# Optimization experiments

Hardware: AMD Instinct MI355X
Metric: run time of the kernel (lower is better)

## Reference

```python
import jax, jax.numpy as jnp
import numpy as np

WIN = 7


def rel_index(win: int) -> jnp.ndarray:
    ys, xs = jnp.meshgrid(jnp.arange(win), jnp.arange(win), indexing='ij')
    coords = jnp.stack([ys.reshape(-1), xs.reshape(-1)], axis=-1)  # (S, 2)
    diff = coords[None, :, :] - coords[:, None, :] + (win - 1)     # (S, S, 2)
    return diff[..., 0] * (2 * win - 1) + diff[..., 1]             # (S, S)


def setup_inputs() -> dict:
    key = jax.random.key(0)
    ks = jax.random.split(key, 5)
    B, WN, S, C, H = 64, 64, WIN * WIN, 192, 6
    X = jax.random.normal(ks[0], (B, WN, S, C), dtype=jnp.float32)
    # torch nn.Linear(emb_dim, 3*emb_dim) -> store as (in, out) for x @ W
    Wqkv = jax.random.normal(ks[1], (C, 3 * C), dtype=jnp.float32) * 0.02
    bqkv = jnp.zeros((3 * C,), dtype=jnp.float32)
    Wo = jax.random.normal(ks[2], (C, C), dtype=jnp.float32) * 0.02
    bo = jnp.zeros((C,), dtype=jnp.float32)
    bias_table = jax.random.normal(ks[3], ((2 * WIN - 1) ** 2, H), dtype=jnp.float32) * 0.02
    return {"X": X, "Wqkv": Wqkv, "bqkv": bqkv, "Wo": Wo, "bo": bo, "bias_table": bias_table}


def reference(X, Wqkv, bqkv, Wo, bo, bias_table):
    B, WN, S, C = X.shape
    H = bias_table.shape[1]
    D = C // H
    scale = D ** -0.5
    # qkv projection: (B, WN, S, 3C) -> (3, B, WN, H, S, D)
    qkv = (X @ Wqkv + bqkv).reshape(B, WN, S, 3, H, D).transpose(3, 0, 1, 4, 2, 5)
    q, k, v = qkv[0], qkv[1], qkv[2]
    attn = jnp.einsum('bwhqd,bwhkd->bwhqk', q, k) * scale  # (B, WN, H, S, S)
    # gathered relative position bias: (S, S, H) -> (H, S, S)
    idx = rel_index(WIN)
    bias = bias_table[idx].transpose(2, 0, 1)
    attn = attn + bias[None, None]
    proba = jax.nn.softmax(attn, axis=-1)  # dropout omitted (eval mode)
    out = jnp.einsum('bwhqk,bwhkd->bwhqd', proba, v)  # (B, WN, H, S, D)
    out = out.transpose(0, 1, 3, 2, 4).reshape(B, WN, S, C)
    return out @ Wo + bo
```

## Files before the change

### kernel.cpp

```cpp
#include <hip/hip_runtime.h>
#include <hip/hip_bf16.h>


typedef __attribute__((ext_vector_type(4))) float f32x4;
typedef __attribute__((ext_vector_type(8))) short bf16x8;
typedef __attribute__((ext_vector_type(4))) unsigned short u16x4;

#define SCALE 0.17677669529663689f
#define MFMA(a, b, acc) __builtin_amdgcn_mfma_f32_16x16x32_bf16(a, b, acc, 0, 0, 0)

__device__ __forceinline__ unsigned short f2bf(float f) {
  union { float f; unsigned int u; } v; v.f = f;
  return (unsigned short)((v.u + 0x7FFFu + ((v.u >> 16) & 1u)) >> 16);
}

__global__ void wprep(const float* __restrict__ Wqkv, const float* __restrict__ Wo,
                      unsigned short* __restrict__ WqkvT, unsigned short* __restrict__ WoT) {
  int i = blockIdx.x * 256 + threadIdx.x;
  if (i < 576 * 192) { int n = i / 192, k = i % 192; WqkvT[i] = f2bf(Wqkv[k * 576 + n]); }
  if (i < 192 * 192) { int n = i / 192, k = i % 192; WoT[i]   = f2bf(Wo[k * 192 + n]); }
}

__global__ __launch_bounds__(512, 4)
void qkv_gemm(const float* __restrict__ X, const unsigned short* __restrict__ WqkvT,
              const float* __restrict__ bqkv, unsigned short* __restrict__ qkv) {
  __shared__ __align__(16) unsigned short Bs[2][64 * 200];
  __shared__ __align__(16) unsigned short scr[8][16 * 72];

  const int tid = threadIdx.x, w8 = tid >> 6, lane = tid & 63;
  const int g = lane >> 4, c = lane & 15;
  const size_t bm = (size_t)blockIdx.x * 128;
  const f32x4 z = {0.f, 0.f, 0.f, 0.f};

  bf16x8 af[6];
  {
    const float* xr = X + (bm + w8 * 16 + c) * 192;
    #pragma unroll
    for (int ks = 0; ks < 6; ++ks) {
      f32x4 lo = *(const f32x4*)(xr + ks * 32 + g * 8);
      f32x4 hi = *(const f32x4*)(xr + ks * 32 + g * 8 + 4);
      bf16x8 a;
      a[0] = (short)f2bf(lo[0]); a[1] = (short)f2bf(lo[1]);
      a[2] = (short)f2bf(lo[2]); a[3] = (short)f2bf(lo[3]);
      a[4] = (short)f2bf(hi[0]); a[5] = (short)f2bf(hi[1]);
      a[6] = (short)f2bf(hi[2]); a[7] = (short)f2bf(hi[3]);
      af[ks] = a;
    }
  }

  uint4 st[3];
  #pragma unroll
  for (int jj = 0; jj < 3; ++jj) {
    int j = tid + jj * 512;
    st[jj] = *(const uint4*)(WqkvT + (j / 24) * 192 + (j % 24) * 8);
  }
  #pragma unroll
  for (int jj = 0; jj < 3; ++jj) {
    int j = tid + jj * 512;
    *(uint4*)(&Bs[0][(j / 24) * 200 + (j % 24) * 8]) = st[jj];
  }
  __syncthreads();

  unsigned short* sw = scr[w8];
  for (int nc = 0; nc < 9; ++nc) {
    const int cur = nc & 1;
    if (nc < 8) {
      #pragma unroll
      for (int jj = 0; jj < 3; ++jj) {
        int j = tid + jj * 512;
        st[jj] = *(const uint4*)(WqkvT + (nc + 1) * 12288 + (j / 24) * 192 + (j % 24) * 8);
      }
    }
    f32x4 acc[4] = {z, z, z, z};
    #pragma unroll
    for (int ks = 0; ks < 6; ++ks) {
      const unsigned short* bp = &Bs[cur][c * 200 + ks * 32 + g * 8];
      #pragma unroll
      for (int nf = 0; nf < 4; ++nf)
        acc[nf] = MFMA(af[ks], *(const bf16x8*)(bp + nf * 16 * 200), acc[nf]);
    }
    #pragma unroll
    for (int nf = 0; nf < 4; ++nf) {
      const float bb = bqkv[nc * 64 + nf * 16 + c];
      #pragma unroll
      for (int r = 0; r < 4; ++r)
        sw[(4 * g + r) * 72 + nf * 16 + c] = f2bf(acc[nf][r] + bb);
    }
    uint4 o0 = *(const uint4*)(sw + c * 72 + g * 8);
    uint4 o1 = *(const uint4*)(sw + c * 72 + 32 + g * 8);
    unsigned short* qp = qkv + (bm + w8 * 16 + c) * 576 + nc * 64;
    *(uint4*)(qp + g * 8)      = o0;
    *(uint4*)(qp + 32 + g * 8) = o1;

    if (nc < 8) {
      #pragma unroll
      for (int jj = 0; jj < 3; ++jj) {
        int j = tid + jj * 512;
        *(uint4*)(&Bs[cur ^ 1][(j / 24) * 200 + (j % 24) * 8]) = st[jj];
      }
    }
    __syncthreads();
  }
}

__global__ __launch_bounds__(512, 4)
void attn_win(unsigned short* __restrict__ qkv, const float* __restrict__ btab) {
  __shared__ __align__(16) unsigned short Ks[64 * 200];
  __shared__ __align__(16) unsigned short Vt[192 * 72];
  __shared__ __align__(16) unsigned short scr[8][1152];
  __shared__ float biasF[1014];

  const int tid = threadIdx.x, w8 = tid >> 6, lane = tid & 63;
  const int g = lane >> 4, c = lane & 15;
  const int mt = w8 & 3, hw = w8 >> 2;
  const size_t tokbase = (size_t)blockIdx.x * 49;
  const f32x4 z = {0.f, 0.f, 0.f, 0.f};

  for (int j = tid; j < 1014; j += 512) biasF[j] = btab[j];
  for (int j = tid; j < 360; j += 512) {
    uint4 zz = {0, 0, 0, 0};
    *(uint4*)(&Ks[(49 + j / 24) * 200 + (j % 24) * 8]) = zz;
  }
  for (int j = tid; j < 2880; j += 512) Vt[(j / 15) * 72 + 49 + j % 15] = 0;
  for (int j = tid; j < 1176; j += 512) {
    int row = j / 24, ch = j % 24;
    *(uint4*)(&Ks[row * 200 + ch * 8]) =
        *(const uint4*)(qkv + (tokbase + row) * 576 + 192 + ch * 8);
  }
  for (int j = tid; j < 1176; j += 512) {
    int row = j / 24, ch = j % 24;
    uint4 v = *(const uint4*)(qkv + (tokbase + row) * 576 + 384 + ch * 8);
    const unsigned short* e = (const unsigned short*)&v;
    #pragma unroll
    for (int k = 0; k < 8; ++k) Vt[(ch * 8 + k) * 72 + row] = e[k];
  }
  __syncthreads();

  const int qbase = mt * 16;
  const int q = qbase + c;
  const bool qvalid = q < 49;
  const int qc = qvalid ? q : 48;
  const int qoff6 = ((6 - qc / 7) * 13 + (6 - qc % 7)) * 6;
  int kb6[16];
  #pragma unroll
  for (int i = 0; i < 16; ++i) {
    int k = (i >> 2) * 16 + g * 4 + (i & 3);
    int kk = k < 49 ? k : 48;
    kb6[i] = ((kk / 7) * 13 + (kk % 7)) * 6;
  }
  unsigned short* Pw = scr[w8];

  for (int hi = 0; hi < 3; ++hi) {
    const int h = hw * 3 + hi;
    const bf16x8 bq = *(const bf16x8*)(qkv + (tokbase + qc) * 576 + h * 32 + g * 8);
    const int cofs = h * 32 + g * 8;
    f32x4 s0 = MFMA(*(const bf16x8*)(Ks + (c) * 200 + cofs), bq, z);
    f32x4 s1 = MFMA(*(const bf16x8*)(Ks + (16 + c) * 200 + cofs), bq, z);
    f32x4 s2 = MFMA(*(const bf16x8*)(Ks + (32 + c) * 200 + cofs), bq, z);
    f32x4 s3 = MFMA(*(const bf16x8*)(Ks + (48 + c) * 200 + cofs), bq, z);

    float p[16];
    float mx = -3e38f;
    #pragma unroll
    for (int i = 0; i < 16; ++i) {
      const int t = i >> 2, r = i & 3;
      const int k = t * 16 + g * 4 + r;
      const float sv = (t == 0) ? s0[r] : (t == 1) ? s1[r] : (t == 2) ? s2[r] : s3[r];
      const float b = biasF[kb6[i] + qoff6 + h];
      const float lg = (qvalid && (k < 49)) ? fmaf(sv, SCALE, b) : -1e30f;
      p[i] = lg;
      mx = fmaxf(mx, lg);
    }
    mx = fmaxf(mx, __shfl_xor(mx, 16));
    mx = fmaxf(mx, __shfl_xor(mx, 32));
    float sum = 0.f;
    #pragma unroll
    for (int i = 0; i < 16; ++i) { p[i] = __expf(p[i] - mx); sum += p[i]; }
    sum += __shfl_xor(sum, 16);
    sum += __shfl_xor(sum, 32);
    const float inv = 1.0f / sum;
    #pragma unroll
    for (int t = 0; t < 4; ++t) {
      u16x4 pk;
      #pragma unroll
      for (int r = 0; r < 4; ++r) pk[r] = f2bf(p[t * 4 + r] * inv);
      *(u16x4*)(Pw + c * 72 + t * 16 + g * 4) = pk;
    }

    f32x4 o0 = z, o1 = z;
    #pragma unroll
    for (int ks = 0; ks < 2; ++ks) {
      const bf16x8 ap = *(const bf16x8*)(Pw + c * 72 + ks * 32 + g * 8);
      const bf16x8 v0 = *(const bf16x8*)(Vt + (h * 32 + c) * 72 + ks * 32 + g * 8);
      const bf16x8 v1 = *(const bf16x8*)(Vt + (h * 32 + 16 + c) * 72 + ks * 32 + g * 8);
      o0 = MFMA(ap, v0, o0);
      o1 = MFMA(ap, v1, o1);
    }
    #pragma unroll
    for (int r = 0; r < 4; ++r) {
      Pw[(4 * g + r) * 72 + c]      = f2bf(o0[r]);
      Pw[(4 * g + r) * 72 + 16 + c] = f2bf(o1[r]);
    }
    uint4 ov = *(const uint4*)(Pw + c * 72 + g * 8);
    if (qvalid)
      *(uint4*)(qkv + (tokbase + q) * 576 + h * 32 + g * 8) = ov;
  }
}

__global__ __launch_bounds__(512, 4)
void out_gemm(const unsigned short* __restrict__ qkv, const unsigned short* __restrict__ WoT,
              const float* __restrict__ bo, float* __restrict__ out) {
  __shared__ __align__(16) unsigned short Ws[192 * 200];

  const int tid = threadIdx.x, w8 = tid >> 6, lane = tid & 63;
  const int g = lane >> 4, c = lane & 15;
  const size_t bm = (size_t)blockIdx.x * 128;
  const f32x4 z = {0.f, 0.f, 0.f, 0.f};

  #pragma unroll
  for (int jj = 0; jj < 9; ++jj) {
    int j = tid + jj * 512;
    *(uint4*)(&Ws[(j / 24) * 200 + (j % 24) * 8]) = *(const uint4*)(WoT + (j / 24) * 192 + (j % 24) * 8);
  }
  __syncthreads();

  bf16x8 af[6];
  #pragma unroll
  for (int ks = 0; ks < 6; ++ks)
    af[ks] = *(const bf16x8*)(qkv + (bm + w8 * 16 + c) * 576 + ks * 32 + g * 8);

  #pragma unroll
  for (int nf = 0; nf < 12; ++nf) {
    const int col = nf * 16 + c;
    const unsigned short* bp = Ws + col * 200;
    f32x4 acc = z;
    #pragma unroll
    for (int ks = 0; ks < 6; ++ks)
      acc = MFMA(af[ks], *(const bf16x8*)(bp + ks * 32 + g * 8), acc);
    const float bb = bo[col];
    #pragma unroll
    for (int r = 0; r < 4; ++r)
      out[(bm + w8 * 16 + 4 * g + r) * 192 + col] = acc[r] + bb;
  }
}

extern "C" void kernel_launch(void* const* d_in, const int* in_sizes, int n_in,
                              void* d_out, int out_size, void* d_ws, size_t ws_size,
                              hipStream_t stream) {
  (void)in_sizes; (void)n_in; (void)out_size; (void)ws_size;
  const float* X    = (const float*)d_in[0];
  const float* Wqkv = (const float*)d_in[1];
  const float* bqkv = (const float*)d_in[2];
  const float* Wo   = (const float*)d_in[3];
  const float* bo   = (const float*)d_in[4];
  const float* btab = (const float*)d_in[5];

  unsigned short* WqkvT = (unsigned short*)d_ws;
  unsigned short* WoT   = WqkvT + 576 * 192;
  unsigned short* qkv   = WoT + 192 * 192;

  wprep<<<432, 256, 0, stream>>>(Wqkv, Wo, WqkvT, WoT);
  qkv_gemm<<<1568, 512, 0, stream>>>(X, WqkvT, bqkv, qkv);
  attn_win<<<4096, 512, 0, stream>>>(qkv, btab);
  out_gemm<<<1568, 512, 0, stream>>>(qkv, WoT, bo, (float*)d_out);
}
```

Baseline: 290.7 us.

## Load swizzled bf16 weights directly into LDS and rotate V transpose stores

Weight preprocessing now writes Wqkv and Wo in an XOR-swizzled bf16 layout. Both GEMM kernels then copy it straight into shared memory with global_load_lds, replacing register-staged copies into padded tiles. The MFMA B-operand reads use the matching XOR index to avoid bank conflicts without padding. The V transpose loop in the attention kernel rotates its element order per chunk to spread LDS bank accesses. This relies on correct ordering of the asynchronous LDS DMA against the barriers.

```diff
diff --git a/kernel.cpp b/kernel.cpp
--- a/kernel.cpp
+++ b/kernel.cpp
@@ -14,18 +14,33 @@
   return (unsigned short)((v.u + 0x7FFFu + ((v.u >> 16) & 1u)) >> 16);
 }
 
+__device__ __forceinline__ void gll16(const unsigned short* src, unsigned short* dst) {
+  __builtin_amdgcn_global_load_lds(
+      (const __attribute__((address_space(1))) unsigned int*)src,
+      (__attribute__((address_space(3))) unsigned int*)dst, 16, 0, 0);
+}
+
 __global__ void wprep(const float* __restrict__ Wqkv, const float* __restrict__ Wo,
-                      unsigned short* __restrict__ WqkvT, unsigned short* __restrict__ WoT) {
+                      unsigned short* __restrict__ WqkvTs, unsigned short* __restrict__ WoTs) {
   int i = blockIdx.x * 256 + threadIdx.x;
-  if (i < 576 * 192) { int n = i / 192, k = i % 192; WqkvT[i] = f2bf(Wqkv[k * 576 + n]); }
-  if (i < 192 * 192) { int n = i / 192, k = i % 192; WoT[i]   = f2bf(Wo[k * 192 + n]); }
+  if (i < 576 * 192) {
+    int n = i / 192, k = i % 192;
+    int ch = n >> 6, row = n & 63;
+    int dst = ch * 12288 + row * 192 + (((k >> 3) ^ (row & 7)) << 3) + (k & 7);
+    WqkvTs[dst] = f2bf(Wqkv[k * 576 + n]);
+  }
+  if (i < 192 * 192) {
+    int n = i / 192, k = i % 192;
+    int dst = n * 192 + (((k >> 3) ^ (n & 7)) << 3) + (k & 7);
+    WoTs[dst] = f2bf(Wo[k * 192 + n]);
+  }
 }
 
 __global__ __launch_bounds__(512, 4)
-void qkv_gemm(const float* __restrict__ X, const unsigned short* __restrict__ WqkvT,
+void qkv_gemm(const float* __restrict__ X, const unsigned short* __restrict__ WqkvTs,
               const float* __restrict__ bqkv, unsigned short* __restrict__ qkv) {
-  __shared__ __align__(16) unsigned short Bs[2][64 * 200];
-  __shared__ __align__(16) unsigned short scr[8][16 * 72];
+  __shared__ __align__(16) unsigned short Bs[2][12288];
+  __shared__ __align__(16) unsigned short scr[8][1152];
 
   const int tid = threadIdx.x, w8 = tid >> 6, lane = tid & 63;
   const int g = lane >> 4, c = lane & 15;
@@ -48,17 +63,9 @@
     }
   }
 
-  uint4 st[3];
-  #pragma unroll
-  for (int jj = 0; jj < 3; ++jj) {
-    int j = tid + jj * 512;
-    st[jj] = *(const uint4*)(WqkvT + (j / 24) * 192 + (j % 24) * 8);
-  }
-  #pragma unroll
-  for (int jj = 0; jj < 3; ++jj) {
-    int j = tid + jj * 512;
-    *(uint4*)(&Bs[0][(j / 24) * 200 + (j % 24) * 8]) = st[jj];
-  }
+  #pragma unroll
+  for (int jj = 0; jj < 3; ++jj)
+    gll16(WqkvTs + (w8 * 3 + jj) * 512 + lane * 8, &Bs[0][(w8 * 3 + jj) * 512]);
   __syncthreads();
 
   unsigned short* sw = scr[w8];
@@ -66,18 +73,19 @@
     const int cur = nc & 1;
     if (nc < 8) {
       #pragma unroll
-      for (int jj = 0; jj < 3; ++jj) {
-        int j = tid + jj * 512;
-        st[jj] = *(const uint4*)(WqkvT + (nc + 1) * 12288 + (j / 24) * 192 + (j % 24) * 8);
+      for (int jj = 0; jj < 3; ++jj)
+        gll16(WqkvTs + (nc + 1) * 12288 + (w8 * 3 + jj) * 512 + lane * 8,
+              &Bs[cur ^ 1][(w8 * 3 + jj) * 512]);
+    }
+    f32x4 acc[4] = {z, z, z, z};
+    #pragma unroll
+    for (int ks = 0; ks < 6; ++ks) {
+      #pragma unroll
+      for (int nf = 0; nf < 4; ++nf) {
+        const bf16x8 bv = *(const bf16x8*)(
+            &Bs[cur][(nf * 16 + c) * 192 + (((ks * 4 + g) ^ (c & 7)) << 3)]);
+        acc[nf] = MFMA(af[ks], bv, acc[nf]);
       }
-    }
-    f32x4 acc[4] = {z, z, z, z};
-    #pragma unroll
-    for (int ks = 0; ks < 6; ++ks) {
-      const unsigned short* bp = &Bs[cur][c * 200 + ks * 32 + g * 8];
-      #pragma unroll
-      for (int nf = 0; nf < 4; ++nf)
-        acc[nf] = MFMA(af[ks], *(const bf16x8*)(bp + nf * 16 * 200), acc[nf]);
     }
     #pragma unroll
     for (int nf = 0; nf < 4; ++nf) {
@@ -91,14 +99,6 @@
     unsigned short* qp = qkv + (bm + w8 * 16 + c) * 576 + nc * 64;
     *(uint4*)(qp + g * 8)      = o0;
     *(uint4*)(qp + 32 + g * 8) = o1;
-
-    if (nc < 8) {
-      #pragma unroll
-      for (int jj = 0; jj < 3; ++jj) {
-        int j = tid + jj * 512;
-        *(uint4*)(&Bs[cur ^ 1][(j / 24) * 200 + (j % 24) * 8]) = st[jj];
-      }
-    }
     __syncthreads();
   }
 }
@@ -132,7 +132,10 @@
     uint4 v = *(const uint4*)(qkv + (tokbase + row) * 576 + 384 + ch * 8);
     const unsigned short* e = (const unsigned short*)&v;
     #pragma unroll
-    for (int k = 0; k < 8; ++k) Vt[(ch * 8 + k) * 72 + row] = e[k];
+    for (int m = 0; m < 8; ++m) {
+      int k = (ch + m) & 7;
+      Vt[(ch * 8 + k) * 72 + row] = e[k];
+    }
   }
   __syncthreads();
 
@@ -181,10 +184,10 @@
     const float inv = 1.0f / sum;
     #pragma unroll
     for (int t = 0; t < 4; ++t) {
-      u16x4 pk;
-      #pragma unroll
-      for (int r = 0; r < 4; ++r) pk[r] = f2bf(p[t * 4 + r] * inv);
-      *(u16x4*)(Pw + c * 72 + t * 16 + g * 4) = pk;
+      u16x4 pkv;
+      #pragma unroll
+      for (int r = 0; r < 4; ++r) pkv[r] = f2bf(p[t * 4 + r] * inv);
+      *(u16x4*)(Pw + c * 72 + t * 16 + g * 4) = pkv;
     }
 
     f32x4 o0 = z, o1 = z;
@@ -208,9 +211,9 @@
 }
 
 __global__ __launch_bounds__(512, 4)
-void out_gemm(const unsigned short* __restrict__ qkv, const unsigned short* __restrict__ WoT,
+void out_gemm(const unsigned short* __restrict__ qkv, const unsigned short* __restrict__ WoTs,
               const float* __restrict__ bo, float* __restrict__ out) {
-  __shared__ __align__(16) unsigned short Ws[192 * 200];
+  __shared__ __align__(16) unsigned short Ws[192 * 192];
 
   const int tid = threadIdx.x, w8 = tid >> 6, lane = tid & 63;
   const int g = lane >> 4, c = lane & 15;
@@ -218,25 +221,25 @@
   const f32x4 z = {0.f, 0.f, 0.f, 0.f};
 
   #pragma unroll
-  for (int jj = 0; jj < 9; ++jj) {
-    int j = tid + jj * 512;
-    *(uint4*)(&Ws[(j / 24) * 200 + (j % 24) * 8]) = *(const uint4*)(WoT + (j / 24) * 192 + (j % 24) * 8);
-  }
-  __syncthreads();
+  for (int jj = 0; jj < 9; ++jj)
+    gll16(WoTs + (w8 * 9 + jj) * 512 + lane * 8, &Ws[(w8 * 9 + jj) * 512]);
 
   bf16x8 af[6];
   #pragma unroll
   for (int ks = 0; ks < 6; ++ks)
     af[ks] = *(const bf16x8*)(qkv + (bm + w8 * 16 + c) * 576 + ks * 32 + g * 8);
+  __syncthreads();
 
   #pragma unroll
   for (int nf = 0; nf < 12; ++nf) {
     const int col = nf * 16 + c;
-    const unsigned short* bp = Ws + col * 200;
     f32x4 acc = z;
     #pragma unroll
-    for (int ks = 0; ks < 6; ++ks)
-      acc = MFMA(af[ks], *(const bf16x8*)(bp + ks * 32 + g * 8), acc);
+    for (int ks = 0; ks < 6; ++ks) {
+      const bf16x8 bv = *(const bf16x8*)(
+          &Ws[col * 192 + (((ks * 4 + g) ^ (c & 7)) << 3)]);
+      acc = MFMA(af[ks], bv, acc);
+    }
     const float bb = bo[col];
     #pragma unroll
     for (int r = 0; r < 4; ++r)
@@ -255,12 +258,12 @@
   const float* bo   = (const float*)d_in[4];
   const float* btab = (const float*)d_in[5];
 
-  unsigned short* WqkvT = (unsigned short*)d_ws;
-  unsigned short* WoT   = WqkvT + 576 * 192;
-  unsigned short* qkv   = WoT + 192 * 192;
-
-  wprep<<<432, 256, 0, stream>>>(Wqkv, Wo, WqkvT, WoT);
-  qkv_gemm<<<1568, 512, 0, stream>>>(X, WqkvT, bqkv, qkv);
+  unsigned short* WqkvTs = (unsigned short*)d_ws;
+  unsigned short* WoTs   = WqkvTs + 576 * 192;
+  unsigned short* qkv    = WoTs + 192 * 192;
+
+  wprep<<<432, 256, 0, stream>>>(Wqkv, Wo, WqkvTs, WoTs);
+  qkv_gemm<<<1568, 512, 0, stream>>>(X, WqkvTs, bqkv, qkv);
   attn_win<<<4096, 512, 0, stream>>>(qkv, btab);
-  out_gemm<<<1568, 512, 0, stream>>>(qkv, WoT, bo, (float*)d_out);
-}
+  out_gemm<<<1568, 512, 0, stream>>>(qkv, WoTs, bo, (float*)d_out);
+}
```

Result: no change. 291.5 us (+0.3%).
